# Kernel tuning notes

Hardware: AMD Instinct MI355X
Metric: run time of the kernel (lower is better)

Reference implementation:

```python
import jax, jax.numpy as jnp
import numpy as np

N_NODES = 100000
N_EDGES = 3200000
IN_FEATS = 256
N_UNITS = 32
OUT_FEATS = 40


def setup_inputs() -> dict:
    key = jax.random.key(0)
    k = jax.random.split(key, 6)
    return {
        "x": jax.random.normal(k[0], (N_NODES, IN_FEATS), dtype=jnp.float32),
        "W1": jax.random.normal(k[1], (IN_FEATS, N_UNITS), dtype=jnp.float32) / np.sqrt(IN_FEATS),
        "b1": jnp.zeros((N_UNITS,), dtype=jnp.float32),
        "W2": jax.random.normal(k[2], (N_UNITS, OUT_FEATS), dtype=jnp.float32) / np.sqrt(N_UNITS),
        "b2": jnp.zeros((OUT_FEATS,), dtype=jnp.float32),
        "src": jax.random.randint(k[3], (N_EDGES,), 0, N_NODES, dtype=jnp.int32),
        "dst": jax.random.randint(k[4], (N_EDGES,), 0, N_NODES, dtype=jnp.int32),
    }


def _graph_conv(x, W, b, src, dst, inv_sqrt_out, inv_sqrt_in, n_nodes):
    # DGL GraphConv, norm='both':
    #   out = D_in^{-1/2} * A^T * (D_out^{-1/2} * x @ W) + b
    # Apply the dense transform first (in_feats >= out_feats here) so edge
    # messages are gathered at the narrow width.
    h = (x * inv_sqrt_out[:, None]) @ W              # [N, F_out]
    msgs = h[src]                                     # [E, F_out] gather
    agg = jax.ops.segment_sum(msgs, dst, num_segments=n_nodes)  # [N, F_out]
    return agg * inv_sqrt_in[:, None] + b


def reference(x, W1, b1, W2, b2, src, dst):
    n = x.shape[0]
    ones = jnp.ones((src.shape[0],), dtype=x.dtype)
    out_deg = jax.ops.segment_sum(ones, src, num_segments=n)
    in_deg = jax.ops.segment_sum(ones, dst, num_segments=n)
    inv_sqrt_out = jax.lax.rsqrt(jnp.maximum(out_deg, 1.0))  # DGL clamps deg>=1
    inv_sqrt_in = jax.lax.rsqrt(jnp.maximum(in_deg, 1.0))

    h = _graph_conv(x, W1, b1, src, dst, inv_sqrt_out, inv_sqrt_in, n)
    h = jax.nn.relu(h)
    # dropout(p=0.5, training=False) is identity in eval mode
    h = _graph_conv(h, W2, b2, src, dst, inv_sqrt_out, inv_sqrt_in, n)
    return jax.nn.log_softmax(h, axis=1)
```

## Files before the change

### kernel.cpp

```cpp
#include <hip/hip_runtime.h>
#include <hip/hip_bf16.h>
#include <math.h>

#define N_NODES 100000
#define N_EDGES 3200000
#define IN_FEATS 256
#define N_UNITS 32
#define OUT_FEATS 40

#define NPB 64
#define BSHIFT 6
#define NB 1563
#define CAP 4096

#define NC 49
#define CSHIFT 11
#define CHUNK 8192
#define NBLK ((N_EDGES + CHUNK - 1) / CHUNK)
#define WIN 128

#define GHALF 391
#define NSPLIT (GHALF * 128)

#define ODS 32768
#define ODW 8192
#define OD_NSL 4
#define OD_STR 96
#define HIST_RIDERS (OD_NSL * OD_STR)
#define RED_RIDERS ((N_NODES / 4 + 511) / 512)

__global__ void __launch_bounds__(256) count_kernel(const int* __restrict__ dst,
                                                    int* __restrict__ bucket_count) {
    __shared__ int lh[NB];
    for (int i = threadIdx.x; i < NB; i += 256) lh[i] = 0;
    __syncthreads();
    const int4* d4 = (const int4*)dst;
    const int total4 = N_EDGES / 4;
    for (int i = blockIdx.x * 256 + threadIdx.x; i < total4; i += gridDim.x * 256) {
        int4 v = d4[i];
        atomicAdd(&lh[v.x >> BSHIFT], 1);
        atomicAdd(&lh[v.y >> BSHIFT], 1);
        atomicAdd(&lh[v.z >> BSHIFT], 1);
        atomicAdd(&lh[v.w >> BSHIFT], 1);
    }
    __syncthreads();
    for (int i = threadIdx.x; i < NB; i += 256)
        if (lh[i]) atomicAdd(&bucket_count[i], lh[i]);
}

__global__ void __launch_bounds__(1024) scan_kernel(const int* __restrict__ bucket_count,
                                                    int* __restrict__ gbase,
                                                    int* __restrict__ gcursor,
                                                    int* __restrict__ gbaseA,
                                                    int* __restrict__ gcursorA) {
    __shared__ int ps[1024];
    int t = threadIdx.x;
    int i0 = 2 * t, i1 = 2 * t + 1;
    int a = (i0 < NB) ? bucket_count[i0] : 0;
    int b = (i1 < NB) ? bucket_count[i1] : 0;
    ps[t] = a + b;
    __syncthreads();
    for (int off = 1; off < 1024; off <<= 1) {
        int v = (t >= off) ? ps[t - off] : 0;
        __syncthreads();
        ps[t] += v;
        __syncthreads();
    }
    int excl = ps[t] - (a + b);
    if (i0 < NB) { gbase[i0] = excl; gcursor[i0] = excl; }
    if (i1 <= NB) { gbase[i1] = excl + a; if (i1 < NB) gcursor[i1] = excl + a; }
    __syncthreads();
    if (t < NC) { int v = gbase[t * 32]; gbaseA[t] = v; gcursorA[t] = v; }
    if (t == NC) gbaseA[NC] = N_EDGES;
}

__device__ __forceinline__ void gemm_body(char* smem, int tid, int gblk,
                                          const float* __restrict__ x,
                                          const float* __restrict__ W1,
                                          float* __restrict__ h, int nbase) {
    float* Ws = (float*)smem;
    for (int idx = tid; idx < IN_FEATS * N_UNITS / 4; idx += 512)
        ((float4*)Ws)[idx] = ((const float4*)W1)[idx];
    __syncthreads();
    unsigned n = (unsigned)(nbase + gblk * 128) + (tid >> 2);
    if (n >= (unsigned)N_NODES) return;
    unsigned j0 = (tid & 3) * 8;
    float acc[8] = {0, 0, 0, 0, 0, 0, 0, 0};
    const float4* xr = (const float4*)(x + (size_t)n * IN_FEATS);
    #pragma unroll 4
    for (int k4 = 0; k4 < IN_FEATS / 4; ++k4) {
        float4 xv = xr[k4];
        const float* wk = Ws + (k4 * 4) * N_UNITS + j0;
        #pragma unroll
        for (int jj = 0; jj < 8; ++jj) acc[jj] = fmaf(xv.x, wk[jj], acc[jj]);
        #pragma unroll
        for (int jj = 0; jj < 8; ++jj) acc[jj] = fmaf(xv.y, wk[N_UNITS + jj], acc[jj]);
        #pragma unroll
        for (int jj = 0; jj < 8; ++jj) acc[jj] = fmaf(xv.z, wk[2 * N_UNITS + jj], acc[jj]);
        #pragma unroll
        for (int jj = 0; jj < 8; ++jj) acc[jj] = fmaf(xv.w, wk[3 * N_UNITS + jj], acc[jj]);
    }
    float* hr = h + (size_t)n * N_UNITS + j0;
    #pragma unroll
    for (int jj = 0; jj < 8; ++jj) hr[jj] = acc[jj];
}

__global__ void __launch_bounds__(512) binAgemm_kernel(const int* __restrict__ src,
                                                       const int* __restrict__ dst,
                                                       int* __restrict__ gcursorA,
                                                       unsigned* __restrict__ pairsA,
                                                       const float* __restrict__ x,
                                                       const float* __restrict__ W1,
                                                       float* __restrict__ h,
                                                       unsigned* __restrict__ partials) {
    __shared__ __align__(16) char smem[CHUNK * 4 + 4 * NC * 4];
    int tid = threadIdx.x;
    if (blockIdx.x < GHALF) {
        gemm_body(smem, tid, blockIdx.x, x, W1, h, 0);
        return;
    }
    if (blockIdx.x >= GHALF + NBLK) {
        unsigned* lh = (unsigned*)smem;
        int r = blockIdx.x - (GHALF + NBLK);
        int slice = r / OD_STR;
        int stripe = r % OD_STR;
        for (int i = tid; i < ODW; i += 512) lh[i] = 0;
        __syncthreads();
        int lo = slice * ODS;
        const int4* s4 = (const int4*)src;
        const int total4 = N_EDGES / 4;
        for (int i = stripe * 512 + tid; i < total4; i += OD_STR * 512) {
            int4 v = s4[i];
            unsigned a = (unsigned)(v.x - lo); if (a < ODS) atomicAdd(&lh[a >> 2], 1u << ((a & 3) * 8));
            unsigned b = (unsigned)(v.y - lo); if (b < ODS) atomicAdd(&lh[b >> 2], 1u << ((b & 3) * 8));
            unsigned c = (unsigned)(v.z - lo); if (c < ODS) atomicAdd(&lh[c >> 2], 1u << ((c & 3) * 8));
            unsigned d = (unsigned)(v.w - lo); if (d < ODS) atomicAdd(&lh[d >> 2], 1u << ((d & 3) * 8));
        }
        __syncthreads();
        int4* dstp = (int4*)(partials + (size_t)r * ODW);
        const int4* lh4 = (const int4*)lh;
        for (int i = tid; i < ODW / 4; i += 512) dstp[i] = lh4[i];
        return;
    }
    unsigned* sortedA = (unsigned*)smem;
    int* hist   = (int*)(smem + CHUNK * 4);
    int* lstart = hist + NC;
    int* cur    = lstart + NC;
    int* gres   = cur + NC;
    int e0 = (blockIdx.x - GHALF) * CHUNK;
    int cnt = min(CHUNK, N_EDGES - e0);
    unsigned es[16], ed[16];
    #pragma unroll
    for (int r = 0; r < 16; ++r) {
        int idx = tid + 512 * r;
        if (idx < cnt) { es[r] = src[e0 + idx]; ed[r] = dst[e0 + idx]; }
    }
    if (tid < NC) hist[tid] = 0;
    __syncthreads();
    #pragma unroll
    for (int r = 0; r < 16; ++r) {
        int idx = tid + 512 * r;
        if (idx < cnt) atomicAdd(&hist[ed[r] >> CSHIFT], 1);
    }
    __syncthreads();
    if (tid < 64) {
        int v = (tid < NC) ? hist[tid] : 0;
        int inc = v;
        #pragma unroll
        for (int off = 1; off < 64; off <<= 1) {
            int u = __shfl_up(inc, off, 64);
            if ((tid & 63) >= off) inc += u;
        }
        if (tid < NC) {
            int ls = inc - v;
            lstart[tid] = ls;
            cur[tid] = ls;
            gres[tid] = atomicAdd(&gcursorA[tid], v) - ls;
        }
    }
    __syncthreads();
    #pragma unroll
    for (int r = 0; r < 16; ++r) {
        int idx = tid + 512 * r;
        if (idx < cnt) {
            int c = ed[r] >> CSHIFT;
            int pos = atomicAdd(&cur[c], 1);
            sortedA[pos] = es[r] | ((ed[r] & ((1u << CSHIFT) - 1)) << 17);
        }
    }
    __syncthreads();
    for (int i = tid; i < cnt; i += 512) {
        int lo = 0, hi = NC - 1;
        while (lo < hi) { int mid = (lo + hi + 1) >> 1; if (lstart[mid] <= i) lo = mid; else hi = mid - 1; }
        pairsA[gres[lo] + i] = sortedA[i];
    }
}

__global__ void __launch_bounds__(512) binBgemm_kernel(const unsigned* __restrict__ pairsA,
                                                       const int* __restrict__ gbaseA,
                                                       int* __restrict__ gcursor,
                                                       unsigned* __restrict__ pairs,
                                                       const float* __restrict__ x,
                                                       const float* __restrict__ W1,
                                                       float* __restrict__ h,
                                                       const unsigned* __restrict__ partials,
                                                       float* __restrict__ inv_out) {
    __shared__ __align__(16) char smem[CHUNK * 4 + 4 * WIN * 4 + (NC + 2) * 4];
    int tid = threadIdx.x;
    if (blockIdx.x < GHALF) {
        gemm_body(smem, tid, blockIdx.x, x, W1, h, NSPLIT);
        return;
    }
    if (blockIdx.x >= GHALF + NBLK) {
        int w = (blockIdx.x - (GHALF + NBLK)) * 512 + tid;
        if (w >= N_NODES / 4) return;
        int slice = w >> 13;
        int wloc = w & (ODW - 1);
        const unsigned* p = partials + ((size_t)slice * OD_STR) * ODW + wloc;
        unsigned s = 0;
        #pragma unroll 8
        for (int j = 0; j < OD_STR; ++j) s += p[(size_t)j * ODW];
        float4 r;
        r.x = rsqrtf(fmaxf((float)(s & 0xFF), 1.0f));
        r.y = rsqrtf(fmaxf((float)((s >> 8) & 0xFF), 1.0f));
        r.z = rsqrtf(fmaxf((float)((s >> 16) & 0xFF), 1.0f));
        r.w = rsqrtf(fmaxf((float)(s >> 24), 1.0f));
        *(float4*)(inv_out + 4 * w) = r;
        return;
    }
    unsigned* sortedB = (unsigned*)smem;
    int* hist   = (int*)(smem + CHUNK * 4);
    int* lstart = hist + WIN;
    int* cur    = lstart + WIN;
    int* gres   = cur + WIN;
    int* gA     = gres + WIN;
    if (tid <= NC) gA[tid] = gbaseA[tid];
    if (tid < WIN) hist[tid] = 0;
    int e0 = (blockIdx.x - GHALF) * CHUNK;
    int cnt = min(CHUNK, N_EDGES - e0);
    __syncthreads();
    int c0 = 0;
    { int lo = 0, hi = NC - 1;
      while (lo < hi) { int mid = (lo + hi + 1) >> 1; if (gA[mid] <= e0) lo = mid; else hi = mid - 1; }
      c0 = lo; }
    int w0 = c0 * 32;
    unsigned pv[16]; short fw[16];
    int c = c0;
    #pragma unroll
    for (int r = 0; r < 16; ++r) {
        int idx = tid + 512 * r;
        if (idx < cnt) {
            int pos = e0 + idx;
            while (pos >= gA[c + 1]) ++c;
            unsigned p = pairsA[pos];
            unsigned srcid = p & 0x1FFFF;
            unsigned dl11 = (p >> 17) & 0x7FF;
            int wi = (c - c0) * 32 + (int)(dl11 >> 6);
            atomicAdd(&hist[wi], 1);
            pv[r] = srcid | ((dl11 & 63u) << 24);
            fw[r] = (short)wi;
        }
    }
    __syncthreads();
    if (tid < 64) {
        int v0 = hist[2 * tid], v1 = hist[2 * tid + 1];
        int s = v0 + v1;
        int inc = s;
        #pragma unroll
        for (int off = 1; off < 64; off <<= 1) {
            int u = __shfl_up(inc, off, 64);
            if ((tid & 63) >= off) inc += u;
        }
        int excl = inc - s;
        lstart[2 * tid] = excl;      cur[2 * tid] = excl;
        lstart[2 * tid + 1] = excl + v0; cur[2 * tid + 1] = excl + v0;
        int f0 = w0 + 2 * tid, f1 = f0 + 1;
        gres[2 * tid]     = (f0 < NB) ? (atomicAdd(&gcursor[f0], v0) - excl) : 0;
        gres[2 * tid + 1] = (f1 < NB) ? (atomicAdd(&gcursor[f1], v1) - (excl + v0)) : 0;
    }
    __syncthreads();
    #pragma unroll
    for (int r = 0; r < 16; ++r) {
        int idx = tid + 512 * r;
        if (idx < cnt) {
            int pos = atomicAdd(&cur[fw[r]], 1);
            sortedB[pos] = pv[r];
        }
    }
    __syncthreads();
    for (int i = tid; i < cnt; i += 512) {
        int lo = 0, hi = WIN - 1;
        while (lo < hi) { int mid = (lo + hi + 1) >> 1; if (lstart[mid] <= i) lo = mid; else hi = mid - 1; }
        pairs[gres[lo] + i] = sortedB[i];
    }
}

template <bool LAYER1>
__global__ void __launch_bounds__(256) gather_kernel(
        const float* __restrict__ in, const unsigned* __restrict__ pairs,
        const int* __restrict__ gbase, const float* __restrict__ inv_out,
        const float* __restrict__ b1, float* __restrict__ outbuf,
        float* __restrict__ inv_in) {
    __shared__ int sorted[CAP];
    __shared__ int cnt[NPB];
    __shared__ int start[NPB + 1];
    __shared__ int cur[NPB];
    __shared__ float b1s[N_UNITS];
    int tid = threadIdx.x;
    int b = blockIdx.x;
    int ebeg = gbase[b];
    int ecnt = min(gbase[b + 1] - ebeg, CAP);
    if (tid < NPB) cnt[tid] = 0;
    if (LAYER1 && tid < N_UNITS) b1s[tid] = b1[tid];
    __syncthreads();

    unsigned stash[16];
    #pragma unroll
    for (int r = 0; r < 16; ++r) {
        int idx = tid + 256 * r;
        if (idx < ecnt) {
            unsigned p = pairs[ebeg + idx];
            stash[r] = p;
            atomicAdd(&cnt[p >> 24], 1);
        }
    }
    __syncthreads();

    if (tid < 64) {
        int v = cnt[tid];
        int inc = v;
        #pragma unroll
        for (int off = 1; off < 64; off <<= 1) {
            int u = __shfl_up(inc, off, 64);
            if (tid >= off) inc += u;
        }
        start[tid + 1] = inc;
        cur[tid] = inc - v;
        if (tid == 0) start[0] = 0;
    }
    __syncthreads();

    #pragma unroll
    for (int r = 0; r < 16; ++r) {
        int idx = tid + 256 * r;
        if (idx < ecnt) {
            unsigned p = stash[r];
            int pos = atomicAdd(&cur[p >> 24], 1);
            sorted[pos] = (int)(p & 0xFFFFFF);
        }
    }
    __syncthreads();

    int w = tid >> 6;
    int lane = tid & 63;
    int q = lane & 7;
    int eo = lane >> 3;
    int nd0 = b * NPB;
    #pragma unroll 1
    for (int p = 0; p < 16; ++p) {
        int nd = w * 16 + p;
        int n = nd0 + nd;
        int beg = start[nd];
        int end = start[nd + 1];
        float ax0 = 0.f, ay0 = 0.f, az0 = 0.f, aw0 = 0.f;
        float ax1 = 0.f, ay1 = 0.f, az1 = 0.f, aw1 = 0.f;
        int e = beg + eo;
        for (; e + 8 < end; e += 16) {
            int s0 = sorted[e];
            int s1 = sorted[e + 8];
            float4 v0 = *(const float4*)(in + (size_t)s0 * N_UNITS + q * 4);
            float4 v1 = *(const float4*)(in + (size_t)s1 * N_UNITS + q * 4);
            if (LAYER1) {
                float io0 = inv_out[s0];
                float io1 = inv_out[s1];
                ax0 = fmaf(v0.x, io0, ax0); ay0 = fmaf(v0.y, io0, ay0);
                az0 = fmaf(v0.z, io0, az0); aw0 = fmaf(v0.w, io0, aw0);
                ax1 = fmaf(v1.x, io1, ax1); ay1 = fmaf(v1.y, io1, ay1);
                az1 = fmaf(v1.z, io1, az1); aw1 = fmaf(v1.w, io1, aw1);
            } else {
                ax0 += v0.x; ay0 += v0.y; az0 += v0.z; aw0 += v0.w;
                ax1 += v1.x; ay1 += v1.y; az1 += v1.z; aw1 += v1.w;
            }
        }
        if (e < end) {
            int s0 = sorted[e];
            float4 v = *(const float4*)(in + (size_t)s0 * N_UNITS + q * 4);
            if (LAYER1) {
                float io0 = inv_out[s0];
                ax0 = fmaf(v.x, io0, ax0); ay0 = fmaf(v.y, io0, ay0);
                az0 = fmaf(v.z, io0, az0); aw0 = fmaf(v.w, io0, aw0);
            } else {
                ax0 += v.x; ay0 += v.y; az0 += v.z; aw0 += v.w;
            }
        }
        e += 8;
        if (e < end) {
            int s1 = sorted[e];
            float4 v = *(const float4*)(in + (size_t)s1 * N_UNITS + q * 4);
            if (LAYER1) {
                float io1 = inv_out[s1];
                ax1 = fmaf(v.x, io1, ax1); ay1 = fmaf(v.y, io1, ay1);
                az1 = fmaf(v.z, io1, az1); aw1 = fmaf(v.w, io1, aw1);
            } else {
                ax1 += v.x; ay1 += v.y; az1 += v.z; aw1 += v.w;
            }
        }
        float sx = ax0 + ax1, sy = ay0 + ay1, sz = az0 + az1, sw = aw0 + aw1;
        #pragma unroll
        for (int st = 8; st < 64; st <<= 1) {
            sx += __shfl_xor(sx, st, 64);
            sy += __shfl_xor(sy, st, 64);
            sz += __shfl_xor(sz, st, 64);
            sw += __shfl_xor(sw, st, 64);
        }
        if (eo == 0 && n < N_NODES) {
            if (LAYER1) {
                float ii = rsqrtf(fmaxf((float)(end - beg), 1.0f));
                float io = inv_out[n];
                float4 r;
                r.x = fmaxf(fmaf(sx, ii, b1s[q * 4 + 0]), 0.0f) * io;
                r.y = fmaxf(fmaf(sy, ii, b1s[q * 4 + 1]), 0.0f) * io;
                r.z = fmaxf(fmaf(sz, ii, b1s[q * 4 + 2]), 0.0f) * io;
                r.w = fmaxf(fmaf(sw, ii, b1s[q * 4 + 3]), 0.0f) * io;
                *(float4*)(outbuf + (size_t)n * N_UNITS + q * 4) = r;
                if (q == 0) inv_in[n] = ii;
            } else {
                *(float4*)(outbuf + (size_t)n * N_UNITS + q * 4) =
                    make_float4(sx, sy, sz, sw);
            }
        }
    }
}

__global__ void __launch_bounds__(256) finalize_kernel(
        const float* __restrict__ agg2, const float* __restrict__ inv_in,
        const float* __restrict__ W2, const float* __restrict__ b2,
        float* __restrict__ out, int N) {
    __shared__ float W2s[N_UNITS * OUT_FEATS];
    __shared__ float b2s[OUT_FEATS];
    for (int i = threadIdx.x; i < N_UNITS * OUT_FEATS; i += 256) W2s[i] = W2[i];
    if (threadIdx.x < OUT_FEATS) b2s[threadIdx.x] = b2[threadIdx.x];
    __syncthreads();
    int n = blockIdx.x * 256 + threadIdx.x;
    if (n >= N) return;
    float a[N_UNITS];
    const float4* ar = (const float4*)(agg2 + (size_t)n * N_UNITS);
    #pragma unroll
    for (int qq = 0; qq < N_UNITS / 4; ++qq) {
        float4 v = ar[qq];
        a[qq * 4 + 0] = v.x; a[qq * 4 + 1] = v.y; a[qq * 4 + 2] = v.z; a[qq * 4 + 3] = v.w;
    }
    float ii = inv_in[n];
    float s[OUT_FEATS];
    #pragma unroll
    for (int o = 0; o < OUT_FEATS; ++o) s[o] = 0.0f;
    #pragma unroll
    for (int k = 0; k < N_UNITS; ++k) {
        float ak = a[k];
        #pragma unroll
        for (int o = 0; o < OUT_FEATS; ++o) s[o] = fmaf(ak, W2s[k * OUT_FEATS + o], s[o]);
    }
    float mx = -INFINITY;
    #pragma unroll
    for (int o = 0; o < OUT_FEATS; ++o) {
        s[o] = fmaf(s[o], ii, b2s[o]);
        mx = fmaxf(mx, s[o]);
    }
    float sum = 0.0f;
    #pragma unroll
    for (int o = 0; o < OUT_FEATS; ++o) sum += __expf(s[o] - mx);
    float lse = mx + __logf(sum);
    #pragma unroll
    for (int o = 0; o < OUT_FEATS; ++o) s[o] -= lse;
    float4* orow4 = (float4*)(out + (size_t)n * OUT_FEATS);
    #pragma unroll
    for (int qq = 0; qq < OUT_FEATS / 4; ++qq)
        orow4[qq] = make_float4(s[qq * 4], s[qq * 4 + 1], s[qq * 4 + 2], s[qq * 4 + 3]);
}

extern "C" void kernel_launch(void* const* d_in, const int* in_sizes, int n_in,
                              void* d_out, int out_size, void* d_ws, size_t ws_size,
                              hipStream_t stream) {
    const float* x   = (const float*)d_in[0];
    const float* W1  = (const float*)d_in[1];
    const float* b1  = (const float*)d_in[2];
    const float* W2  = (const float*)d_in[3];
    const float* b2  = (const float*)d_in[4];
    const int*   src = (const int*)d_in[5];
    const int*   dst = (const int*)d_in[6];
    float* out = (float*)d_out;

    char* base = (char*)d_ws;
    float*    inv_out      = (float*)(base);
    int*      bucket_count = (int*)(base + 400000L);
    int*      gbaseA       = (int*)(base + 406400L);
    int*      gcursorA     = (int*)(base + 406912L);
    int*      gbase        = (int*)(base + 408192L);
    int*      gcursor      = (int*)(base + 416384L);
    float*    inv_in       = (float*)(base + 424576L);
    unsigned* pairs        = (unsigned*)(base + 824576L);
    unsigned* pairsA       = (unsigned*)(base + 13624576L);
    float*    rprime       = (float*)(base + 26424576L);
    float*    h            = (float*)(base + 39224576L);
    float*    agg2         = (float*)(base + 39224576L);
    unsigned* partials     = (unsigned*)rprime;

    hipMemsetAsync(bucket_count, 0, 8192L, stream);

    count_kernel<<<128, 256, 0, stream>>>(dst, bucket_count);
    scan_kernel<<<1, 1024, 0, stream>>>(bucket_count, gbase, gcursor, gbaseA, gcursorA);

    binAgemm_kernel<<<GHALF + NBLK + HIST_RIDERS, 512, 0, stream>>>(
        src, dst, gcursorA, pairsA, x, W1, h, partials);
    binBgemm_kernel<<<GHALF + NBLK + RED_RIDERS, 512, 0, stream>>>(
        pairsA, gbaseA, gcursor, pairs, x, W1, h, partials, inv_out);

    gather_kernel<true><<<NB, 256, 0, stream>>>(h, pairs, gbase, inv_out, b1, rprime, inv_in);
    gather_kernel<false><<<NB, 256, 0, stream>>>(rprime, pairs, gbase, inv_out, b1, agg2, inv_in);

    finalize_kernel<<<(N_NODES + 255) / 256, 256, 0, stream>>>(agg2, inv_in, W2, b2, out, N_NODES);
}
```

Baseline: 361.8 us.

## Fold fine bucket histogram into binning pass and drop scan kernel

The fine-bucket count and the single-block scan kernel are replaced by a coarse 49-bin count kernel. Fine bucket counts are now accumulated inside the first binning kernel. Later kernels recompute prefix offsets on the fly with wave shuffles from the coarse and fine counts, using relative cursors. This removes one kernel launch and the serial scan plus a full pass over dst at fine granularity. In exchange it adds redundant per-block prefix computation and more shared-memory atomics in the binning pass.

```diff
diff --git a/kernel.cpp b/kernel.cpp
--- a/kernel.cpp
+++ b/kernel.cpp
@@ -29,49 +29,22 @@
 #define HIST_RIDERS (OD_NSL * OD_STR)
 #define RED_RIDERS ((N_NODES / 4 + 511) / 512)
 
-__global__ void __launch_bounds__(256) count_kernel(const int* __restrict__ dst,
-                                                    int* __restrict__ bucket_count) {
-    __shared__ int lh[NB];
-    for (int i = threadIdx.x; i < NB; i += 256) lh[i] = 0;
+__global__ void __launch_bounds__(256) ccount_kernel(const int* __restrict__ dst,
+                                                     int* __restrict__ ccount) {
+    __shared__ int lh[NC];
+    if (threadIdx.x < NC) lh[threadIdx.x] = 0;
     __syncthreads();
     const int4* d4 = (const int4*)dst;
     const int total4 = N_EDGES / 4;
     for (int i = blockIdx.x * 256 + threadIdx.x; i < total4; i += gridDim.x * 256) {
         int4 v = d4[i];
-        atomicAdd(&lh[v.x >> BSHIFT], 1);
-        atomicAdd(&lh[v.y >> BSHIFT], 1);
-        atomicAdd(&lh[v.z >> BSHIFT], 1);
-        atomicAdd(&lh[v.w >> BSHIFT], 1);
-    }
-    __syncthreads();
-    for (int i = threadIdx.x; i < NB; i += 256)
-        if (lh[i]) atomicAdd(&bucket_count[i], lh[i]);
-}
-
-__global__ void __launch_bounds__(1024) scan_kernel(const int* __restrict__ bucket_count,
-                                                    int* __restrict__ gbase,
-                                                    int* __restrict__ gcursor,
-                                                    int* __restrict__ gbaseA,
-                                                    int* __restrict__ gcursorA) {
-    __shared__ int ps[1024];
-    int t = threadIdx.x;
-    int i0 = 2 * t, i1 = 2 * t + 1;
-    int a = (i0 < NB) ? bucket_count[i0] : 0;
-    int b = (i1 < NB) ? bucket_count[i1] : 0;
-    ps[t] = a + b;
-    __syncthreads();
-    for (int off = 1; off < 1024; off <<= 1) {
-        int v = (t >= off) ? ps[t - off] : 0;
-        __syncthreads();
-        ps[t] += v;
-        __syncthreads();
-    }
-    int excl = ps[t] - (a + b);
-    if (i0 < NB) { gbase[i0] = excl; gcursor[i0] = excl; }
-    if (i1 <= NB) { gbase[i1] = excl + a; if (i1 < NB) gcursor[i1] = excl + a; }
-    __syncthreads();
-    if (t < NC) { int v = gbase[t * 32]; gbaseA[t] = v; gcursorA[t] = v; }
-    if (t == NC) gbaseA[NC] = N_EDGES;
+        atomicAdd(&lh[v.x >> CSHIFT], 1);
+        atomicAdd(&lh[v.y >> CSHIFT], 1);
+        atomicAdd(&lh[v.z >> CSHIFT], 1);
+        atomicAdd(&lh[v.w >> CSHIFT], 1);
+    }
+    __syncthreads();
+    if (threadIdx.x < NC && lh[threadIdx.x]) atomicAdd(&ccount[threadIdx.x], lh[threadIdx.x]);
 }
 
 __device__ __forceinline__ void gemm_body(char* smem, int tid, int gblk,
@@ -105,15 +78,26 @@
     for (int jj = 0; jj < 8; ++jj) hr[jj] = acc[jj];
 }
 
+#define BA_SORT 0
+#define BA_HIST (CHUNK * 4)
+#define BA_LST  (BA_HIST + NC * 4)
+#define BA_CUR  (BA_LST + NC * 4)
+#define BA_GRES (BA_CUR + NC * 4)
+#define BA_CB   (BA_GRES + NC * 4)
+#define BA_LHF  (BA_CB + (NC + 1) * 4)
+#define BA_SMEM (BA_LHF + ((NB + 3) & ~3) * 4)
+
 __global__ void __launch_bounds__(512) binAgemm_kernel(const int* __restrict__ src,
                                                        const int* __restrict__ dst,
+                                                       const int* __restrict__ ccount,
+                                                       int* __restrict__ bucket_count,
                                                        int* __restrict__ gcursorA,
                                                        unsigned* __restrict__ pairsA,
                                                        const float* __restrict__ x,
                                                        const float* __restrict__ W1,
                                                        float* __restrict__ h,
                                                        unsigned* __restrict__ partials) {
-    __shared__ __align__(16) char smem[CHUNK * 4 + 4 * NC * 4];
+    __shared__ __align__(16) char smem[BA_SMEM];
     int tid = threadIdx.x;
     if (blockIdx.x < GHALF) {
         gemm_body(smem, tid, blockIdx.x, x, W1, h, 0);
@@ -142,11 +126,13 @@
         for (int i = tid; i < ODW / 4; i += 512) dstp[i] = lh4[i];
         return;
     }
-    unsigned* sortedA = (unsigned*)smem;
-    int* hist   = (int*)(smem + CHUNK * 4);
-    int* lstart = hist + NC;
-    int* cur    = lstart + NC;
-    int* gres   = cur + NC;
+    unsigned* sortedA = (unsigned*)(smem + BA_SORT);
+    int* hist   = (int*)(smem + BA_HIST);
+    int* lstart = (int*)(smem + BA_LST);
+    int* cur    = (int*)(smem + BA_CUR);
+    int* gres   = (int*)(smem + BA_GRES);
+    int* cbaseS = (int*)(smem + BA_CB);
+    int* lhf    = (int*)(smem + BA_LHF);
     int e0 = (blockIdx.x - GHALF) * CHUNK;
     int cnt = min(CHUNK, N_EDGES - e0);
     unsigned es[16], ed[16];
@@ -156,11 +142,26 @@
         if (idx < cnt) { es[r] = src[e0 + idx]; ed[r] = dst[e0 + idx]; }
     }
     if (tid < NC) hist[tid] = 0;
+    for (int i = tid; i < NB; i += 512) lhf[i] = 0;
+    if (tid < 64) {
+        int v = (tid < NC) ? ccount[tid] : 0;
+        int inc = v;
+        #pragma unroll
+        for (int off = 1; off < 64; off <<= 1) {
+            int u = __shfl_up(inc, off, 64);
+            if (tid >= off) inc += u;
+        }
+        if (tid < NC) cbaseS[tid] = inc - v;
+        if (tid == NC) cbaseS[NC] = N_EDGES;
+    }
     __syncthreads();
     #pragma unroll
     for (int r = 0; r < 16; ++r) {
         int idx = tid + 512 * r;
-        if (idx < cnt) atomicAdd(&hist[ed[r] >> CSHIFT], 1);
+        if (idx < cnt) {
+            atomicAdd(&hist[ed[r] >> CSHIFT], 1);
+            atomicAdd(&lhf[ed[r] >> BSHIFT], 1);
+        }
     }
     __syncthreads();
     if (tid < 64) {
@@ -175,7 +176,7 @@
             int ls = inc - v;
             lstart[tid] = ls;
             cur[tid] = ls;
-            gres[tid] = atomicAdd(&gcursorA[tid], v) - ls;
+            gres[tid] = cbaseS[tid] + atomicAdd(&gcursorA[tid], v) - ls;
         }
     }
     __syncthreads();
@@ -194,18 +195,29 @@
         while (lo < hi) { int mid = (lo + hi + 1) >> 1; if (lstart[mid] <= i) lo = mid; else hi = mid - 1; }
         pairsA[gres[lo] + i] = sortedA[i];
     }
-}
+    for (int i = tid; i < NB; i += 512)
+        if (lhf[i]) atomicAdd(&bucket_count[i], lhf[i]);
+}
+
+#define BB_SORT 0
+#define BB_HIST (CHUNK * 4)
+#define BB_LST  (BB_HIST + WIN * 4)
+#define BB_CUR  (BB_LST + WIN * 4)
+#define BB_GRES (BB_CUR + WIN * 4)
+#define BB_CB   (BB_GRES + WIN * 4)
+#define BB_SMEM (BB_CB + (NC + 2) * 4)
 
 __global__ void __launch_bounds__(512) binBgemm_kernel(const unsigned* __restrict__ pairsA,
-                                                       const int* __restrict__ gbaseA,
-                                                       int* __restrict__ gcursor,
+                                                       const int* __restrict__ ccount,
+                                                       const int* __restrict__ bucket_count,
+                                                       int* __restrict__ gcur_rel,
                                                        unsigned* __restrict__ pairs,
                                                        const float* __restrict__ x,
                                                        const float* __restrict__ W1,
                                                        float* __restrict__ h,
                                                        const unsigned* __restrict__ partials,
                                                        float* __restrict__ inv_out) {
-    __shared__ __align__(16) char smem[CHUNK * 4 + 4 * WIN * 4 + (NC + 2) * 4];
+    __shared__ __align__(16) char smem[BB_SMEM];
     int tid = threadIdx.x;
     if (blockIdx.x < GHALF) {
         gemm_body(smem, tid, blockIdx.x, x, W1, h, NSPLIT);
@@ -228,14 +240,24 @@
         *(float4*)(inv_out + 4 * w) = r;
         return;
     }
-    unsigned* sortedB = (unsigned*)smem;
-    int* hist   = (int*)(smem + CHUNK * 4);
-    int* lstart = hist + WIN;
-    int* cur    = lstart + WIN;
-    int* gres   = cur + WIN;
-    int* gA     = gres + WIN;
-    if (tid <= NC) gA[tid] = gbaseA[tid];
-    if (tid < WIN) hist[tid] = 0;
+    unsigned* sortedB = (unsigned*)(smem + BB_SORT);
+    int* hist   = (int*)(smem + BB_HIST);
+    int* lstart = (int*)(smem + BB_LST);
+    int* cur    = (int*)(smem + BB_CUR);
+    int* gres   = (int*)(smem + BB_GRES);
+    int* gA     = (int*)(smem + BB_CB);
+    if (tid < 64) {
+        int v = (tid < NC) ? ccount[tid] : 0;
+        int inc = v;
+        #pragma unroll
+        for (int off = 1; off < 64; off <<= 1) {
+            int u = __shfl_up(inc, off, 64);
+            if (tid >= off) inc += u;
+        }
+        if (tid < NC) gA[tid] = inc - v;
+        if (tid == NC) gA[NC] = N_EDGES;
+    }
+    if (tid >= 64 && tid < 64 + WIN) hist[tid - 64] = 0;
     int e0 = (blockIdx.x - GHALF) * CHUNK;
     int cnt = min(CHUNK, N_EDGES - e0);
     __syncthreads();
@@ -275,8 +297,20 @@
         lstart[2 * tid] = excl;      cur[2 * tid] = excl;
         lstart[2 * tid + 1] = excl + v0; cur[2 * tid + 1] = excl + v0;
         int f0 = w0 + 2 * tid, f1 = f0 + 1;
-        gres[2 * tid]     = (f0 < NB) ? (atomicAdd(&gcursor[f0], v0) - excl) : 0;
-        gres[2 * tid + 1] = (f1 < NB) ? (atomicAdd(&gcursor[f1], v1) - (excl + v0)) : 0;
+        int bc0 = (f0 < NB) ? bucket_count[f0] : 0;
+        int bc1 = (f1 < NB) ? bucket_count[f1] : 0;
+        int ps = bc0 + bc1;
+        int pinc = ps;
+        #pragma unroll
+        for (int off = 1; off < 16; off <<= 1) {
+            int u = __shfl_up(pinc, off, 64);
+            if ((tid & 15) >= off) pinc += u;
+        }
+        int pexcl = pinc - ps;
+        int creg = (w0 >> 5) + (tid >> 4);
+        int gb0 = gA[creg < NC ? creg : NC] + pexcl;
+        gres[2 * tid]     = (f0 < NB) ? (gb0 + atomicAdd(&gcur_rel[f0], v0) - excl) : 0;
+        gres[2 * tid + 1] = (f1 < NB) ? (gb0 + bc0 + atomicAdd(&gcur_rel[f1], v1) - (excl + v0)) : 0;
     }
     __syncthreads();
     #pragma unroll
@@ -298,7 +332,8 @@
 template <bool LAYER1>
 __global__ void __launch_bounds__(256) gather_kernel(
         const float* __restrict__ in, const unsigned* __restrict__ pairs,
-        const int* __restrict__ gbase, const float* __restrict__ inv_out,
+        const int* __restrict__ ccount, const int* __restrict__ bucket_count,
+        const float* __restrict__ inv_out,
         const float* __restrict__ b1, float* __restrict__ outbuf,
         float* __restrict__ inv_in) {
     __shared__ int sorted[CAP];
@@ -306,13 +341,27 @@
     __shared__ int start[NPB + 1];
     __shared__ int cur[NPB];
     __shared__ float b1s[N_UNITS];
+    __shared__ int ebeg_s, ecnt_s;
     int tid = threadIdx.x;
     int b = blockIdx.x;
-    int ebeg = gbase[b];
-    int ecnt = min(gbase[b + 1] - ebeg, CAP);
     if (tid < NPB) cnt[tid] = 0;
     if (LAYER1 && tid < N_UNITS) b1s[tid] = b1[tid];
-    __syncthreads();
+    if (tid < 64) {
+        int reg = b >> 5;
+        int base32 = b & ~31;
+        int val = 0;
+        if (tid < reg) val = ccount[tid];
+        if (tid < (b & 31)) {
+            int fb = base32 + tid;
+            if (fb < NB) val += bucket_count[fb];
+        }
+        #pragma unroll
+        for (int st = 1; st < 64; st <<= 1) val += __shfl_xor(val, st, 64);
+        if (tid == 0) { ebeg_s = val; ecnt_s = min(bucket_count[b], CAP); }
+    }
+    __syncthreads();
+    int ebeg = ebeg_s;
+    int ecnt = ecnt_s;
 
     unsigned stash[16];
     #pragma unroll
@@ -492,11 +541,10 @@
 
     char* base = (char*)d_ws;
     float*    inv_out      = (float*)(base);
-    int*      bucket_count = (int*)(base + 400000L);
-    int*      gbaseA       = (int*)(base + 406400L);
-    int*      gcursorA     = (int*)(base + 406912L);
-    int*      gbase        = (int*)(base + 408192L);
-    int*      gcursor      = (int*)(base + 416384L);
+    int*      ccount       = (int*)(base + 400000L);
+    int*      bucket_count = (int*)(base + 400256L);
+    int*      gcursorA     = (int*)(base + 406528L);
+    int*      gcur_rel     = (int*)(base + 406784L);
     float*    inv_in       = (float*)(base + 424576L);
     unsigned* pairs        = (unsigned*)(base + 824576L);
     unsigned* pairsA       = (unsigned*)(base + 13624576L);
@@ -505,18 +553,19 @@
     float*    agg2         = (float*)(base + 39224576L);
     unsigned* partials     = (unsigned*)rprime;
 
-    hipMemsetAsync(bucket_count, 0, 8192L, stream);
-
-    count_kernel<<<128, 256, 0, stream>>>(dst, bucket_count);
-    scan_kernel<<<1, 1024, 0, stream>>>(bucket_count, gbase, gcursor, gbaseA, gcursorA);
+    hipMemsetAsync(base + 400000L, 0, 13056L, stream);
+
+    ccount_kernel<<<128, 256, 0, stream>>>(dst, ccount);
 
     binAgemm_kernel<<<GHALF + NBLK + HIST_RIDERS, 512, 0, stream>>>(
-        src, dst, gcursorA, pairsA, x, W1, h, partials);
+        src, dst, ccount, bucket_count, gcursorA, pairsA, x, W1, h, partials);
     binBgemm_kernel<<<GHALF + NBLK + RED_RIDERS, 512, 0, stream>>>(
-        pairsA, gbaseA, gcursor, pairs, x, W1, h, partials, inv_out);
-
-    gather_kernel<true><<<NB, 256, 0, stream>>>(h, pairs, gbase, inv_out, b1, rprime, inv_in);
-    gather_kernel<false><<<NB, 256, 0, stream>>>(rprime, pairs, gbase, inv_out, b1, agg2, inv_in);
+        pairsA, ccount, bucket_count, gcur_rel, pairs, x, W1, h, partials, inv_out);
+
+    gather_kernel<true><<<NB, 256, 0, stream>>>(h, pairs, ccount, bucket_count,
+                                                inv_out, b1, rprime, inv_in);
+    gather_kernel<false><<<NB, 256, 0, stream>>>(rprime, pairs, ccount, bucket_count,
+                                                 inv_out, b1, agg2, inv_in);
 
     finalize_kernel<<<(N_NODES + 255) / 256, 256, 0, stream>>>(agg2, inv_in, W2, b2, out, N_NODES);
 }
```

Result: no change. 363.3 us (+0.4%).
